# Kernel optimization log

Measured on AMD Instinct MI355X. Metric: run time of the kernel, lower is better.

The kernel has to match this reference:

```python
import jax, jax.numpy as jnp
import numpy as np

L, B, CIN, H, W = 32, 4, 3, 16, 16
D, HEADS, DK, DEPTH = 64, 4, 16, 2
EPS = 1e-5
BN_INV = float(1.0 / np.sqrt(1.0 + EPS))  # eval-mode BatchNorm with default stats/affine


def conv2d(x, w, b=None, pad=1, groups=1):
    y = jax.lax.conv_general_dilated(
        x, w, window_strides=(1, 1), padding=[(pad, pad), (pad, pad)],
        dimension_numbers=('NCHW', 'OIHW', 'NCHW'), feature_group_count=groups)
    if b is not None:
        y = y + b[None, :, None, None]
    return y


def layer_norm(x, w, b):
    # LayerNorm over last 3 dims [D,H,W] of (L,B,D,H,W)
    mu = jnp.mean(x, axis=(-3, -2, -1), keepdims=True)
    var = jnp.var(x, axis=(-3, -2, -1), keepdims=True)
    return (x - mu) * jax.lax.rsqrt(var + EPS) * w + b


def pos_table():
    pos = jnp.arange(L, dtype=jnp.float32)
    exp = (2.0 * (jnp.arange(D) // 2).astype(jnp.float32)) / D
    angle = pos[:, None] / jnp.power(10000.0, exp)[None, :]  # (L, D)
    # source applies sin to even POSITIONS and cos to odd POSITIONS (table[0::2]=sin)
    tab = jnp.where((jnp.arange(L) % 2 == 0)[:, None], jnp.sin(angle), jnp.cos(angle))
    return tab[:, None, :, None, None]  # (L,1,D,1,1) broadcast over B,H,W


def reference(x, gw1, gb1, gw2, gb2, gw3, gb3, gw4, gb4,
              conv1_w, conv1_b, conv2_w, conv2_b, wq, wk, wv, w0,
              ln1_w, ln1_b, ln2_w, ln2_b, ff_w1, ff_b1, ff_w2, ff_b2):
    lrelu = lambda v: jax.nn.leaky_relu(v, 0.01)
    h = x.reshape(L * B, CIN, H, W)
    for w_, b_ in ((gw1, gb1), (gw2, gb2), (gw3, gb3), (gw4, gb4)):
        h = lrelu(conv2d(h, w_, b_) * BN_INV)
    xlb = h.reshape(L, B, D, H, W) + pos_table()

    for i in range(DEPTH):
        # ---- multi-head conv attention (dec=True) ----
        y = layer_norm(xlb, ln1_w[i], ln1_b[i])
        xa = jnp.transpose(y, (1, 2, 3, 4, 0))  # (B,D,H,W,L)
        # conv1 is a 1x1 conv == pointwise linear over channels, per head
        qkv = jnp.einsum('bchwl,noc->bnohwl', xa, conv1_w[i]) \
            + conv1_b[i][None, :, :, None, None, None]  # (B,HEADS,3D,H,W,L)
        q, k, v = jnp.split(qkv, 3, axis=2)  # each (B,HEADS,D,H,W,L)
        q = jnp.einsum('bnchwl,nck->bnkhwl', q, wq[i])  # (B,HEADS,DK,H,W,L)
        k = jnp.einsum('bnchwl,nck->bnkhwl', k, wk[i])
        v = jnp.einsum('bnchwl,nck->bnkhwl', v, wv[i])

        def head_conv(t):
            # 5x5 conv per head (no bias): conv2(Q_i + K_j) = conv_w(Q)_i + conv_w(K)_j + bias
            z = jnp.transpose(t, (0, 5, 1, 2, 3, 4)).reshape(B * L, HEADS * DK, H, W)
            z = conv2d(z, conv2_w[i].reshape(HEADS * DK, DK, 5, 5), None, pad=2, groups=HEADS)
            return jnp.transpose(z.reshape(B, L, HEADS, DK, H, W), (0, 2, 3, 4, 5, 1))

        cq = head_conv(q)
        ck = head_conv(k)
        logits = cq[..., :, None] + ck[..., None, :] \
            + conv2_b[i][None, :, :, None, None, None, None]  # (B,HEADS,DK,H,W,Lq,Lk)
        a = jax.nn.softmax(logits, axis=-1)
        vout = jnp.einsum('bnkhwij,bnkhwj->bnkhwi', a, v)   # (B,HEADS,DK,H,W,L)
        vcat = vout.reshape(B, D, H, W, L)                  # concat heads on channel dim
        attn = jnp.einsum('bchwl,co->bohwl', vcat, w0[i])
        xlb = xlb + jnp.transpose(attn, (4, 0, 1, 2, 3))

        # ---- feed-forward over the TIME dimension (Linear on L) ----
        y = layer_norm(xlb, ln2_w[i], ln2_b[i])
        xp = jnp.transpose(y, (1, 2, 3, 4, 0))  # (B,D,H,W,L)
        h1 = lrelu(jnp.einsum('bchwl,ml->bchwm', xp, ff_w1[i]) + ff_b1[i])
        ff = jnp.einsum('bchwm,lm->bchwl', h1, ff_w2[i]) + ff_b2[i]
        xlb = xlb + jnp.transpose(ff, (4, 0, 1, 2, 3))
    return xlb


def setup_inputs() -> dict:
    key = jax.random.key(0)
    specs = {
        'x': (L, B, CIN, H, W),
        'gw1': (4, 3, 3, 3), 'gb1': (4,), 'gw2': (6, 4, 3, 3), 'gb2': (6,),
        'gw3': (8, 6, 3, 3), 'gb3': (8,), 'gw4': (64, 8, 3, 3), 'gb4': (64,),
        'conv1_w': (DEPTH, HEADS, 3 * D, D), 'conv1_b': (DEPTH, HEADS, 3 * D),
        'conv2_w': (DEPTH, HEADS, DK, DK, 5, 5), 'conv2_b': (DEPTH, HEADS, DK),
        'wq': (DEPTH, HEADS, D, DK), 'wk': (DEPTH, HEADS, D, DK), 'wv': (DEPTH, HEADS, D, DK),
        'w0': (DEPTH, D, D),
        'ln1_w': (DEPTH, D, H, W), 'ln1_b': (DEPTH, D, H, W),
        'ln2_w': (DEPTH, D, H, W), 'ln2_b': (DEPTH, D, H, W),
        'ff_w1': (DEPTH, 4 * L, L), 'ff_b1': (DEPTH, 4 * L),
        'ff_w2': (DEPTH, L, 4 * L), 'ff_b2': (DEPTH, L),
    }
    out = {}
    for idx, (name, shape) in enumerate(specs.items()):
        g = jax.random.normal(jax.random.fold_in(key, idx), shape, dtype=jnp.float32)
        if name == 'x':
            out[name] = g
        elif name in ('ln1_w', 'ln2_w'):
            out[name] = 1.0 + 0.05 * g
        else:
            out[name] = 0.05 * g
    return out
```

## Files before the change

kernel.cpp:

```cpp
#include <hip/hip_runtime.h>
#include <math.h>

#define LL 32
#define BB 4
#define DD 64
#define NH 4
#define DKK 16
#define BN_INV 0.9999950000374997f

__device__ __forceinline__ float lrelu(float v){ return v > 0.f ? v : 0.01f*v; }

__global__ void k_eff(const float* __restrict__ c1w, const float* __restrict__ c1b,
                      const float* __restrict__ wk, const float* __restrict__ wv,
                      float* __restrict__ A, float* __restrict__ bf){
  int tid = blockIdx.x*256 + threadIdx.x;
  int k = tid & 15, d = (tid>>4)&63, n=(tid>>10)&3, t=(tid>>12)&1, i=tid>>13;
  const float* wsel = (t ? wv : wk) + (i*NH+n)*64*16;
  const float* cw   = c1w + ((i*NH+n)*192 + (t+1)*64)*64;
  float acc = 0.f;
  for(int c=0;c<64;++c) acc += cw[c*64+d]*wsel[c*16+k];
  A[tid] = acc;
  if(d==0){
    const float* cb = c1b + (i*NH+n)*192 + (t+1)*64;
    float ba=0.f;
    for(int c=0;c<64;++c) ba += cb[c]*wsel[c*16+k];
    bf[((i*2+t)*4+n)*16+k] = ba;
  }
}

__global__ void k_pos(float* __restrict__ pos){
  int tid = blockIdx.x*256 + threadIdx.x;
  int d = tid & 63, l = tid >> 6;
  float ex = (float)(d>>1) / 32.0f;
  float angle = (float)l * powf(10000.0f, -ex);
  pos[tid] = (l & 1) ? cosf(angle) : sinf(angle);
}

__global__ void k_wT(const float* __restrict__ w2, float* __restrict__ wT){
  int tid = blockIdx.x*256 + threadIdx.x;
  int k = tid & 15; int rest = tid >> 4;
  int tap = rest % 25; int rest2 = rest / 25;
  int c = rest2 & 15; int dn = rest2 >> 4;
  wT[tid] = w2[((dn*16 + k)*16 + c)*25 + tap];
}

__global__ void k_wT3(const float* __restrict__ gw4, float* __restrict__ wT3){
  int tid = blockIdx.x*256 + threadIdx.x;
  if(tid >= 4608) return;
  int co = tid & 63, ct = tid >> 6;
  wT3[ct*64 + co] = gw4[co*72 + ct];
}

__global__ __launch_bounds__(256) void k_front(const float* __restrict__ x,
    const float* __restrict__ gw1, const float* __restrict__ gb1,
    const float* __restrict__ gw2, const float* __restrict__ gb2,
    const float* __restrict__ gw3, const float* __restrict__ gb3,
    float* __restrict__ out8){
  __shared__ float sh[4212];
  float* T0 = sh; float* T1 = sh + 972; float* T2 = sh + 2268;
  int f = blockIdx.x, t = threadIdx.x;
  int h = t>>4, w = t&15;
  for(int j=t;j<4212;j+=256) sh[j]=0.f;
  __syncthreads();
  for(int ci=0;ci<3;++ci) T0[ci*324 + (h+1)*18 + (w+1)] = x[f*768 + ci*256 + t];
  __syncthreads();
  for(int co=0;co<4;++co){
    float acc = gb1[co];
    for(int ci=0;ci<3;++ci){
      const float* tb = T0 + ci*324 + h*18 + w;
      const float* wb = gw1 + co*27 + ci*9;
      #pragma unroll
      for(int dy=0;dy<3;++dy)
        #pragma unroll
        for(int dx=0;dx<3;++dx) acc += tb[dy*18+dx]*wb[dy*3+dx];
    }
    T1[co*324 + (h+1)*18 + (w+1)] = lrelu(acc*BN_INV);
  }
  __syncthreads();
  for(int co=0;co<6;++co){
    float acc = gb2[co];
    for(int ci=0;ci<4;++ci){
      const float* tb = T1 + ci*324 + h*18 + w;
      const float* wb = gw2 + co*36 + ci*9;
      #pragma unroll
      for(int dy=0;dy<3;++dy)
        #pragma unroll
        for(int dx=0;dx<3;++dx) acc += tb[dy*18+dx]*wb[dy*3+dx];
    }
    T2[co*324 + (h+1)*18 + (w+1)] = lrelu(acc*BN_INV);
  }
  __syncthreads();
  for(int co=0;co<8;++co){
    float acc = gb3[co];
    for(int ci=0;ci<6;++ci){
      const float* tb = T2 + ci*324 + h*18 + w;
      const float* wb = gw3 + co*54 + ci*9;
      #pragma unroll
      for(int dy=0;dy<3;++dy)
        #pragma unroll
        for(int dx=0;dx<3;++dx) acc += tb[dy*18+dx]*wb[dy*3+dx];
    }
    out8[f*2048 + co*256 + t] = lrelu(acc*BN_INV);
  }
}

__global__ __launch_bounds__(256) void k_conv3_l4(const float* __restrict__ in8,
    const float* __restrict__ wT3, const float* __restrict__ gb4,
    const float* __restrict__ pos, float* __restrict__ out){
  __shared__ float tile[8*324];
  __shared__ float wsl[1152];
  int blk = blockIdx.x; int g = blk & 3; int f = blk >> 2;
  int t = threadIdx.x; int h = t>>4, w = t&15;
  for(int j=t;j<2592;j+=256) tile[j]=0.f;
  for(int j=t;j<1152;j+=256){
    int ct = j>>4, c16 = j&15;
    wsl[j] = wT3[ct*64 + g*16 + c16];
  }
  __syncthreads();
  for(int ci=0;ci<8;++ci) tile[ci*324 + (h+1)*18 + (w+1)] = in8[f*2048 + ci*256 + t];
  __syncthreads();
  float acc[16];
  #pragma unroll
  for(int q=0;q<16;++q) acc[q] = gb4[g*16+q];
  for(int ci=0;ci<8;++ci){
    const float* tb = tile + ci*324 + h*18 + w;
    #pragma unroll
    for(int dy=0;dy<3;++dy){
      #pragma unroll
      for(int dx=0;dx<3;++dx){
        float v = tb[dy*18+dx];
        const float* wp = wsl + (ci*9+dy*3+dx)*16;
        float4 wa = *(const float4*)(wp);
        float4 wb = *(const float4*)(wp+4);
        float4 wc = *(const float4*)(wp+8);
        float4 wd = *(const float4*)(wp+12);
        acc[0]+=v*wa.x; acc[1]+=v*wa.y; acc[2]+=v*wa.z; acc[3]+=v*wa.w;
        acc[4]+=v*wb.x; acc[5]+=v*wb.y; acc[6]+=v*wb.z; acc[7]+=v*wb.w;
        acc[8]+=v*wc.x; acc[9]+=v*wc.y; acc[10]+=v*wc.z; acc[11]+=v*wc.w;
        acc[12]+=v*wd.x; acc[13]+=v*wd.y; acc[14]+=v*wd.z; acc[15]+=v*wd.w;
      }
    }
  }
  int l = f >> 2;
  #pragma unroll
  for(int q=0;q<16;++q){
    float r = lrelu(acc[q]*BN_INV) + pos[l*64 + g*16 + q];
    out[f*16384 + (g*16+q)*256 + t] = r;
  }
}

__global__ __launch_bounds__(1024) void k_ln(const float* __restrict__ x,
                     const float* __restrict__ w, const float* __restrict__ b,
                     float* __restrict__ y){
  int g = blockIdx.x, t = threadIdx.x;
  const float4* xb = (const float4*)(x + g*16384);
  float4 xv[4];
  float s=0.f, s2=0.f;
  #pragma unroll
  for(int j=0;j<4;++j){
    float4 v = xb[t + j*1024];
    xv[j] = v;
    s  += v.x + v.y + v.z + v.w;
    s2 += v.x*v.x + v.y*v.y + v.z*v.z + v.w*v.w;
  }
  __shared__ float ls[1024], ls2[1024];
  ls[t]=s; ls2[t]=s2; __syncthreads();
  for(int off=512;off>0;off>>=1){
    if(t<off){ ls[t]+=ls[t+off]; ls2[t]+=ls2[t+off]; }
    __syncthreads();
  }
  float mu  = ls[0]*(1.0f/16384.f);
  float var = ls2[0]*(1.0f/16384.f) - mu*mu;
  float rinv = rsqrtf(var + 1e-5f);
  const float4* wb = (const float4*)w;
  const float4* bb = (const float4*)b;
  float4* yb = (float4*)(y + g*16384);
  #pragma unroll
  for(int j=0;j<4;++j){
    int e = t + j*1024;
    float4 v = xv[j], wv = wb[e], bv = bb[e], o;
    o.x = (v.x-mu)*rinv*wv.x + bv.x;
    o.y = (v.y-mu)*rinv*wv.y + bv.y;
    o.z = (v.z-mu)*rinv*wv.z + bv.z;
    o.w = (v.w-mu)*rinv*wv.w + bv.w;
    yb[e] = o;
  }
}

__global__ __launch_bounds__(256) void k_kv(const float* __restrict__ y,
                     const float* __restrict__ A, const float* __restrict__ bf,
                     float* __restrict__ K, float* __restrict__ V, int dep){
  int blk = blockIdx.x;
  int n = blk & 3; int lb = blk >> 2;
  int t = threadIdx.x;
  const float* yb  = y + lb*16384 + t;
  const float* akb = A + ((dep*2+0)*4+n)*1024;
  const float* avb = A + ((dep*2+1)*4+n)*1024;
  float kacc[16], vacc[16];
  #pragma unroll
  for(int q=0;q<16;++q){
    kacc[q] = bf[((dep*2+0)*4+n)*16+q];
    vacc[q] = bf[((dep*2+1)*4+n)*16+q];
  }
  for(int d=0;d<64;++d){
    float yv = yb[d*256];
    const float* ak = akb + d*16;
    const float* av = avb + d*16;
    #pragma unroll
    for(int q=0;q<16;++q){ kacc[q] += yv*ak[q]; vacc[q] += yv*av[q]; }
  }
  int l = lb >> 2, b = lb & 3;
  int base = ((b*32+l)*4+n)*4096 + t;
  #pragma unroll
  for(int q=0;q<16;++q){ K[base + q*256] = kacc[q]; V[base + q*256] = vacc[q]; }
}

__global__ __launch_bounds__(256) void k_conv5(const float* __restrict__ K,
                       const float* __restrict__ wT, float* __restrict__ CK, int dep){
  __shared__ float tile[16*400];
  int blk = blockIdx.x;
  int khalf = blk & 1; int fh = blk >> 1; int n = fh & 3;
  int t = threadIdx.x;
  const float* kb = K + fh*4096;
  for(int j=t;j<6400;j+=256) tile[j]=0.f;
  __syncthreads();
  int h = t>>4, w = t&15;
  for(int c=0;c<16;++c) tile[c*400 + (h+2)*20 + (w+2)] = kb[c*256+t];
  __syncthreads();
  const float* wb = wT + (dep*4+n)*6400 + khalf*8;
  float acc[8] = {0.f,0.f,0.f,0.f,0.f,0.f,0.f,0.f};
  for(int c=0;c<16;++c){
    const float* tb = tile + c*400 + h*20 + w;
    const float* wc = wb + c*400;
    #pragma unroll
    for(int dy=0;dy<5;++dy){
      #pragma unroll
      for(int dx=0;dx<5;++dx){
        float v = tb[dy*20+dx];
        const float* wp = wc + (dy*5+dx)*16;
        float4 wa = *(const float4*)(wp);
        float4 wbv = *(const float4*)(wp+4);
        acc[0]+=v*wa.x; acc[1]+=v*wa.y; acc[2]+=v*wa.z; acc[3]+=v*wa.w;
        acc[4]+=v*wbv.x; acc[5]+=v*wbv.y; acc[6]+=v*wbv.z; acc[7]+=v*wbv.w;
      }
    }
  }
  float* ob = CK + fh*4096 + khalf*8*256;
  #pragma unroll
  for(int q=0;q<8;++q) ob[q*256+t] = acc[q];
}

__global__ void k_soft(const float* __restrict__ CK, const float* __restrict__ V,
                       float* __restrict__ vout){
  int idx = blockIdx.x*256 + threadIdx.x;
  int p = idx&255; int k=(idx>>8)&15; int n=(idx>>12)&3; int b=idx>>14;
  int base = (b*128 + n)*4096 + k*256 + p;
  float e[32]; float m = -1e30f;
  for(int l=0;l<32;++l){ float v = CK[base + l*16384]; e[l]=v; m = fmaxf(m,v); }
  float s = 0.f;
  for(int l=0;l<32;++l){ e[l] = expf(e[l]-m); s += e[l]; }
  float inv = 1.f/s, acc = 0.f;
  for(int l=0;l<32;++l) acc += e[l]*V[base + l*16384];
  vout[((b*4+n)*16+k)*256+p] = acc*inv;
}

__global__ void k_w0res(const float* __restrict__ vout, const float* __restrict__ w0,
                        float* __restrict__ xlb, int dep){
  int idx = blockIdx.x*256 + threadIdx.x;
  int p = idx&255; int o=(idx>>8)&63; int b=idx>>14;
  const float* vb = vout + b*64*256 + p;
  const float* wb = w0 + dep*4096 + o;
  float acc = 0.f;
  for(int c=0;c<64;++c) acc += vb[c*256]*wb[c*64];
  for(int l=0;l<32;++l) xlb[((l*4+b)*64+o)*256 + p] += acc;
}

__global__ __launch_bounds__(256, 4) void k_ff(const float* __restrict__ y,
                     const float* __restrict__ w1, const float* __restrict__ b1,
                     const float* __restrict__ w2, const float* __restrict__ b2,
                     float* __restrict__ xlb, int dep){
  __shared__ float w1s[32*32];
  __shared__ float w2s[32*32];
  int blk = blockIdx.x;
  int mg = blk & 3; int qblk = blk >> 2;
  int t = threadIdx.x;
  const float* w1b = w1 + dep*4096 + mg*32*32;
  const float* w2b = w2 + dep*4096 + mg*32;
  #pragma unroll
  for(int j=0;j<4;++j){
    int e = t + j*256;
    w1s[e] = w1b[e];
    int l = e >> 5, mm = e & 31;
    w2s[e] = w2b[l*128 + mm];
  }
  __syncthreads();
  int base = qblk*256 + t;
  float yv[32];
  #pragma unroll
  for(int l=0;l<32;++l) yv[l] = y[base + l*65536];
  float fa[32];
  if(mg==0){
    #pragma unroll
    for(int l=0;l<32;++l) fa[l] = b2[dep*32+l];
  } else {
    #pragma unroll
    for(int l=0;l<32;++l) fa[l] = 0.f;
  }
  const float* b1b = b1 + dep*128 + mg*32;
  for(int mm=0;mm<32;++mm){
    float s = b1b[mm];
    #pragma unroll
    for(int l=0;l<32;++l) s += yv[l]*w1s[mm*32+l];
    s = lrelu(s);
    #pragma unroll
    for(int l=0;l<32;++l) fa[l] += s*w2s[l*32+mm];
  }
  #pragma unroll
  for(int l=0;l<32;++l) atomicAdd(&xlb[base + l*65536], fa[l]);
}

extern "C" void kernel_launch(void* const* d_in, const int* in_sizes, int n_in,
                              void* d_out, int out_size, void* d_ws, size_t ws_size,
                              hipStream_t stream) {
  const float* x       = (const float*)d_in[0];
  const float* gw1     = (const float*)d_in[1];
  const float* gb1     = (const float*)d_in[2];
  const float* gw2     = (const float*)d_in[3];
  const float* gb2     = (const float*)d_in[4];
  const float* gw3     = (const float*)d_in[5];
  const float* gb3     = (const float*)d_in[6];
  const float* gw4     = (const float*)d_in[7];
  const float* gb4     = (const float*)d_in[8];
  const float* conv1_w = (const float*)d_in[9];
  const float* conv1_b = (const float*)d_in[10];
  const float* conv2_w = (const float*)d_in[11];
  const float* wk      = (const float*)d_in[14];
  const float* wv      = (const float*)d_in[15];
  const float* w0      = (const float*)d_in[16];
  const float* ln1_w   = (const float*)d_in[17];
  const float* ln1_b   = (const float*)d_in[18];
  const float* ln2_w   = (const float*)d_in[19];
  const float* ln2_b   = (const float*)d_in[20];
  const float* ff_w1   = (const float*)d_in[21];
  const float* ff_b1   = (const float*)d_in[22];
  const float* ff_w2   = (const float*)d_in[23];
  const float* ff_b2   = (const float*)d_in[24];

  float* out = (float*)d_out;
  float* ws  = (float*)d_ws;
  float* Y    = ws;
  float* K    = ws + 2097152;
  float* CK   = ws + 4194304;
  float* V    = ws + 6291456;
  float* vout = ws + 8388608;
  float* A    = ws + 8454144;
  float* bf   = ws + 8470528;
  float* pos  = ws + 8470784;
  float* wT   = ws + 8472832;
  float* wT3  = ws + 8524032;

  k_eff<<<64, 256, 0, stream>>>(conv1_w, conv1_b, wk, wv, A, bf);
  k_pos<<<8, 256, 0, stream>>>(pos);
  k_wT <<<200, 256, 0, stream>>>(conv2_w, wT);
  k_wT3<<<18, 256, 0, stream>>>(gw4, wT3);

  k_front   <<<128, 256, 0, stream>>>(x, gw1, gb1, gw2, gb2, gw3, gb3, K);
  k_conv3_l4<<<512, 256, 0, stream>>>(K, wT3, gb4, pos, out);

  for(int dep=0; dep<2; ++dep){
    k_ln   <<<128, 1024, 0, stream>>>(out, ln1_w + dep*16384, ln1_b + dep*16384, Y);
    k_kv   <<<512,  256, 0, stream>>>(Y, A, bf, K, V, dep);
    k_conv5<<<1024, 256, 0, stream>>>(K, wT, CK, dep);
    k_soft <<<256,  256, 0, stream>>>(CK, V, vout);
    k_w0res<<<256,  256, 0, stream>>>(vout, w0, out, dep);
    k_ln   <<<128, 1024, 0, stream>>>(out, ln2_w + dep*16384, ln2_b + dep*16384, Y);
    k_ff   <<<1024, 256, 0, stream>>>(Y, ff_w1, ff_b1, ff_w2, ff_b2, out, dep);
  }
}
```

Baseline: 359.9 us.

## Compute full feed-forward hidden dimension per thread, dropping atomics and shared staging

The feed-forward kernel previously split the 128 hidden units into four groups across blocks, staged weights in shared memory and merged partial results with atomicAdd into the residual. Now each thread processes all 128 hidden units for one spatial position, reads weights directly from global memory as uniform loads, and does a plain read-modify-write on the residual. This removes atomic traffic and the extra reads of the input, at the cost of 4x fewer blocks (256) and a longer serial loop per thread, which may reduce latency hiding. Per-thread work also grows, and the dot product now uses split accumulators to shorten the dependency chain.

```diff
diff --git a/kernel.cpp b/kernel.cpp
--- a/kernel.cpp
+++ b/kernel.cpp
@@ -275,48 +275,36 @@
   for(int l=0;l<32;++l) xlb[((l*4+b)*64+o)*256 + p] += acc;
 }
 
-__global__ __launch_bounds__(256, 4) void k_ff(const float* __restrict__ y,
+__global__ __launch_bounds__(256) void k_ff(const float* __restrict__ y,
                      const float* __restrict__ w1, const float* __restrict__ b1,
                      const float* __restrict__ w2, const float* __restrict__ b2,
                      float* __restrict__ xlb, int dep){
-  __shared__ float w1s[32*32];
-  __shared__ float w2s[32*32];
-  int blk = blockIdx.x;
-  int mg = blk & 3; int qblk = blk >> 2;
-  int t = threadIdx.x;
-  const float* w1b = w1 + dep*4096 + mg*32*32;
-  const float* w2b = w2 + dep*4096 + mg*32;
-  #pragma unroll
-  for(int j=0;j<4;++j){
-    int e = t + j*256;
-    w1s[e] = w1b[e];
-    int l = e >> 5, mm = e & 31;
-    w2s[e] = w2b[l*128 + mm];
-  }
-  __syncthreads();
-  int base = qblk*256 + t;
+  int idx = blockIdx.x*256 + threadIdx.x;
   float yv[32];
   #pragma unroll
-  for(int l=0;l<32;++l) yv[l] = y[base + l*65536];
+  for(int l=0;l<32;++l) yv[l] = y[idx + l*65536];
   float fa[32];
-  if(mg==0){
-    #pragma unroll
-    for(int l=0;l<32;++l) fa[l] = b2[dep*32+l];
-  } else {
-    #pragma unroll
-    for(int l=0;l<32;++l) fa[l] = 0.f;
-  }
-  const float* b1b = b1 + dep*128 + mg*32;
-  for(int mm=0;mm<32;++mm){
-    float s = b1b[mm];
-    #pragma unroll
-    for(int l=0;l<32;++l) s += yv[l]*w1s[mm*32+l];
-    s = lrelu(s);
-    #pragma unroll
-    for(int l=0;l<32;++l) fa[l] += s*w2s[l*32+mm];
-  }
-  #pragma unroll
-  for(int l=0;l<32;++l) atomicAdd(&xlb[base + l*65536], fa[l]);
+  #pragma unroll
+  for(int l=0;l<32;++l) fa[l] = b2[dep*32+l];
+  const float* w1b = w1 + dep*4096;
+  const float* w2b = w2 + dep*4096;
+  const float* b1b = b1 + dep*128;
+  #pragma unroll 4
+  for(int m=0;m<128;++m){
+    float s0=0.f,s1=0.f,s2=0.f,s3=0.f;
+    #pragma unroll
+    for(int l=0;l<32;l+=4){
+      s0 += yv[l+0]*w1b[m*32+l+0];
+      s1 += yv[l+1]*w1b[m*32+l+1];
+      s2 += yv[l+2]*w1b[m*32+l+2];
+      s3 += yv[l+3]*w1b[m*32+l+3];
+    }
+    float s = lrelu(((s0+s1)+(s2+s3)) + b1b[m]);
+    #pragma unroll
+    for(int l=0;l<32;++l) fa[l] += s*w2b[l*128+m];
+  }
+  #pragma unroll
+  for(int l=0;l<32;++l) xlb[idx + l*65536] += fa[l];
 }
 
 extern "C" void kernel_launch(void* const* d_in, const int* in_sizes, int n_in,
@@ -374,6 +362,6 @@
     k_soft <<<256,  256, 0, stream>>>(CK, V, vout);
     k_w0res<<<256,  256, 0, stream>>>(vout, w0, out, dep);
     k_ln   <<<128, 1024, 0, stream>>>(out, ln2_w + dep*16384, ln2_b + dep*16384, Y);
-    k_ff   <<<1024, 256, 0, stream>>>(Y, ff_w1, ff_b1, ff_w2, ff_b2, out, dep);
-  }
-}
+    k_ff   <<<256,  256, 0, stream>>>(Y, ff_w1, ff_b1, ff_w2, ff_b2, out, dep);
+  }
+}
```

Measured after the change: 495.5 us. 37.7% more time.
